# Performance work log

Hardware: AMD Instinct MI355X
Metric: run time of the kernel (lower is better)

The kernel has to match this reference:

```python
import jax, jax.numpy as jnp
import numpy as np

S, B, D, H = 2048, 64, 128, 128


def setup_inputs() -> dict:
    key = jax.random.key(0)
    ks = jax.random.split(key, 7)
    scale = 1.0 / np.sqrt(H)
    return {
        "input": jax.random.normal(ks[0], (S, B, D), dtype=jnp.float32),
        "time": jax.random.uniform(ks[1], (S, B, 1), dtype=jnp.float32),
        "W_ih": jax.random.normal(ks[2], (4 * H, D), dtype=jnp.float32) * scale,
        "W_hh": jax.random.normal(ks[3], (4 * H, H), dtype=jnp.float32) * scale,
        "b": jax.random.normal(ks[4], (4 * H,), dtype=jnp.float32) * scale,
        "w_t": jax.random.uniform(ks[5], (H,), dtype=jnp.float32),
        "b_t": jax.random.uniform(ks[6], (H,), dtype=jnp.float32),
    }


def reference(input, time, W_ih, W_hh, b, w_t, b_t):
    # ReverseLSTMLayer: run a time-conditioned LSTM cell over REVERSED time steps,
    # then re-reverse the stacked outputs. state starts at zeros (state=None).
    Bsz = input.shape[1]
    Hd = W_hh.shape[1]

    def step(state, xt):
        x, t = xt  # x: [B, D], t: [B, 1]
        h, c = state
        gates = x @ W_ih.T + h @ W_hh.T + b  # [B, 4H]
        i_, f_, g_, o_ = jnp.split(gates, 4, axis=-1)
        i_ = jax.nn.sigmoid(i_)
        f_ = jax.nn.sigmoid(f_)
        g_ = jnp.tanh(g_)
        o_ = jax.nn.sigmoid(o_)
        # learned exponential time decay on the carried cell state (T-LSTM style)
        decay = jnp.exp(-jax.nn.relu(t * w_t + b_t))  # [B, H]
        c = f_ * c * decay + i_ * g_
        h = o_ * jnp.tanh(c)
        return (h, c), h

    init = (jnp.zeros((Bsz, Hd), input.dtype), jnp.zeros((Bsz, Hd), input.dtype))
    # iterate over reversed sequence, then reverse outputs back
    (h, c), ys_rev = jax.lax.scan(step, init, (input[::-1], time[::-1]))
    outputs = ys_rev[::-1]  # [S, B, H]
    return outputs, (h, c)
```

## Files before the change

kernel.cpp:

```cpp
#include <hip/hip_runtime.h>

#define S_LEN 2048
#define B_SZ  64
#define D_IN  128
#define H_SZ  128
#define G4    512

typedef __attribute__((ext_vector_type(4))) float     floatx4;
typedef __attribute__((ext_vector_type(8))) _Float16  half8;
typedef __attribute__((ext_vector_type(2))) _Float16  half2_t;

union H8 { half8 v; half2_t p[4]; };

template<int CTRL>
__device__ __forceinline__ float qperm(float v) {
  return __int_as_float(
      __builtin_amdgcn_mov_dpp(__float_as_int(v), CTRL, 0xF, 0xF, true));
}

__global__ __launch_bounds__(256) void gx_gemm(
    const float* __restrict__ X,
    const float* __restrict__ Wih,
    const float* __restrict__ bias,
    _Float16* __restrict__ gx)
{
  __shared__ _Float16 Wl[128][136];
  const int tid  = threadIdx.x;
  const int lane = tid & 63;
  const int wv   = tid >> 6;
  const int R0   = blockIdx.x * 64;
  const int m    = lane & 15;
  const int q    = lane >> 4;

  half8 afrag[4];
  const float* xrow = X + (size_t)(R0 + wv * 16 + m) * D_IN;
  #pragma unroll
  for (int kf = 0; kf < 4; ++kf) {
    const int k0 = kf * 32 + q * 8;
    floatx4 v0 = *(const floatx4*)(xrow + k0);
    floatx4 v1 = *(const floatx4*)(xrow + k0 + 4);
    half8 a;
    a[0] = (_Float16)v0.x; a[1] = (_Float16)v0.y;
    a[2] = (_Float16)v0.z; a[3] = (_Float16)v0.w;
    a[4] = (_Float16)v1.x; a[5] = (_Float16)v1.y;
    a[6] = (_Float16)v1.z; a[7] = (_Float16)v1.w;
    afrag[kf] = a;
  }

  for (int nc = 0; nc < 4; ++nc) {
    __syncthreads();
    for (int i = tid; i < 128 * 32; i += 256) {
      const int row = i >> 5;
      const int c4  = (i & 31) * 4;
      floatx4 v = *(const floatx4*)(Wih + ((size_t)nc * 128 + row) * D_IN + c4);
      Wl[row][c4 + 0] = (_Float16)v.x;
      Wl[row][c4 + 1] = (_Float16)v.y;
      Wl[row][c4 + 2] = (_Float16)v.z;
      Wl[row][c4 + 3] = (_Float16)v.w;
    }
    __syncthreads();

    #pragma unroll
    for (int nt = 0; nt < 8; ++nt) {
      const int n0  = nc * 128 + nt * 16;
      const int nlo = nt * 16 + m;
      const float bv = bias[n0 + m];
      floatx4 acc = {bv, bv, bv, bv};
      #pragma unroll
      for (int kf = 0; kf < 4; ++kf) {
        half8 bfrag = *(const half8*)(&Wl[nlo][kf * 32 + q * 8]);
        acc = __builtin_amdgcn_mfma_f32_16x16x32_f16(afrag[kf], bfrag, acc,
                                                     0, 0, 0);
      }
      _Float16* gp = gx + (size_t)(R0 + wv * 16 + q * 4) * G4 + n0 + m;
      #pragma unroll
      for (int r = 0; r < 4; ++r) gp[(size_t)r * G4] = (_Float16)acc[r];
    }
  }
}

__global__ __launch_bounds__(512, 2) void lstm_rev(
    const _Float16* __restrict__ gx,
    const float* __restrict__ timep,
    const float* __restrict__ Whh,
    const float* __restrict__ w_t,
    const float* __restrict__ b_t,
    float* __restrict__ out)
{
  __shared__ __align__(16) _Float16 hbuf[2][H_SZ];
  const int tid = threadIdx.x;
  const int b   = blockIdx.x;
  const int tt  = tid & 3;
  const int col = tid >> 2;
  const int j   = tt * 128 + col;

  half8 w[4][4];
  #pragma unroll
  for (int ty = 0; ty < 4; ++ty) {
    const float* wrow = Whh + (size_t)(ty * 128 + col) * H_SZ + tt * 8;
    #pragma unroll
    for (int i = 0; i < 4; ++i) {
      floatx4 v0 = *(const floatx4*)(wrow + i * 32);
      floatx4 v1 = *(const floatx4*)(wrow + i * 32 + 4);
      half8 hh;
      hh[0] = (_Float16)v0.x; hh[1] = (_Float16)v0.y;
      hh[2] = (_Float16)v0.z; hh[3] = (_Float16)v0.w;
      hh[4] = (_Float16)v1.x; hh[5] = (_Float16)v1.y;
      hh[6] = (_Float16)v1.z; hh[7] = (_Float16)v1.w;
      w[ty][i] = hh;
    }
  }

  const float wt = w_t[col];
  const float bt = b_t[col];

  if (tid < H_SZ) hbuf[0][tid] = (_Float16)0.0f;
  __syncthreads();

  const float LOG2E  = 1.4426950408889634f;
  const float kscale = (tt == 2) ? (-2.0f * LOG2E) : (-LOG2E);
  const float am     = (tt == 2) ? 2.0f : 1.0f;
  const float aa     = (tt == 2) ? -1.0f : 0.0f;
  const bool  odd    = (tt & 1) != 0;

  float c = 0.0f;
  {
    const size_t idx0 = (size_t)(S_LEN - 1) * B_SZ + b;
    float gxc = (float)gx[idx0 * G4 + j];
    float tmc = timep[idx0];

    for (int t = S_LEN - 1; t >= 0; --t) {
      const int tn = (t > 0) ? (t - 1) : 0;
      const size_t idxn = (size_t)tn * B_SZ + b;
      const float gxn = (float)gx[idxn * G4 + j];
      const float tmn = timep[idxn];

      const int rb = (S_LEN - 1 - t) & 1;

      H8 hv[4];
      #pragma unroll
      for (int i = 0; i < 4; ++i)
        hv[i].v = *(const half8*)(&hbuf[rb][i * 32 + tt * 8]);

      float acc[4][2] = {{0.f,0.f},{0.f,0.f},{0.f,0.f},{0.f,0.f}};
      #pragma unroll
      for (int i = 0; i < 4; ++i) {
        H8 wu0; wu0.v = w[0][i];
        H8 wu1; wu1.v = w[1][i];
        H8 wu2; wu2.v = w[2][i];
        H8 wu3; wu3.v = w[3][i];
        #pragma unroll
        for (int p = 0; p < 4; ++p) {
          const int ch = p >> 1;
          acc[0][ch] = __builtin_amdgcn_fdot2(hv[i].p[p], wu0.p[p],
                                              acc[0][ch], false);
          acc[1][ch] = __builtin_amdgcn_fdot2(hv[i].p[p], wu1.p[p],
                                              acc[1][ch], false);
          acc[2][ch] = __builtin_amdgcn_fdot2(hv[i].p[p], wu2.p[p],
                                              acc[2][ch], false);
          acc[3][ch] = __builtin_amdgcn_fdot2(hv[i].p[p], wu3.p[p],
                                              acc[3][ch], false);
        }
      }
      float a0 = acc[0][0] + acc[0][1];
      float a1 = acc[1][0] + acc[1][1];
      float a2 = acc[2][0] + acc[2][1];
      float a3 = acc[3][0] + acc[3][1];

      a0 += qperm<0xB1>(a0); a0 += qperm<0x4E>(a0);
      a1 += qperm<0xB1>(a1); a1 += qperm<0x4E>(a1);
      a2 += qperm<0xB1>(a2); a2 += qperm<0x4E>(a2);
      a3 += qperm<0xB1>(a3); a3 += qperm<0x4E>(a3);

      float pre = (tt & 1) ? ((tt & 2) ? a3 : a1) : ((tt & 2) ? a2 : a0);
      pre += gxc;

      const float e = __builtin_amdgcn_exp2f(pre * kscale);
      const float v = fmaf(am, __builtin_amdgcn_rcpf(1.0f + e), aa);

      float z = fmaf(tmc, wt, bt);
      z = fmaxf(z, 0.0f);
      const float d = __builtin_amdgcn_exp2f(-LOG2E * z);

      const float p2 = qperm<0x4E>(v);
      const float fv = (tt == 1) ? v : p2;
      const float r  = odd ? fv * (d * c) : v * p2;
      const float cn = r + qperm<0xB1>(r);
      c = cn;

      const float e2 = __builtin_amdgcn_exp2f(-2.0f * LOG2E * cn);
      const float th = fmaf(2.0f, __builtin_amdgcn_rcpf(1.0f + e2), -1.0f);

      if (tt == 3) {
        const float h = v * th;
        hbuf[rb ^ 1][col] = (_Float16)h;
        out[((size_t)t * B_SZ + b) * H_SZ + col] = h;
        if (t == 0) {
          out[(size_t)S_LEN * B_SZ * H_SZ + (size_t)b * H_SZ + col] = h;
          out[(size_t)S_LEN * B_SZ * H_SZ + (size_t)B_SZ * H_SZ
              + (size_t)b * H_SZ + col] = c;
        }
      }
      __syncthreads();
      gxc = gxn; tmc = tmn;
    }
  }
}

extern "C" void kernel_launch(void* const* d_in, const int* in_sizes, int n_in,
                              void* d_out, int out_size, void* d_ws, size_t ws_size,
                              hipStream_t stream) {
  const float* input = (const float*)d_in[0];
  const float* timep = (const float*)d_in[1];
  const float* W_ih  = (const float*)d_in[2];
  const float* W_hh  = (const float*)d_in[3];
  const float* bias  = (const float*)d_in[4];
  const float* w_t   = (const float*)d_in[5];
  const float* b_t   = (const float*)d_in[6];
  float* out = (float*)d_out;

  _Float16* gx = (_Float16*)d_ws;

  gx_gemm<<<dim3((S_LEN * B_SZ) / 64), dim3(256), 0, stream>>>(
      input, W_ih, bias, gx);

  lstm_rev<<<dim3(B_SZ), dim3(512), 0, stream>>>(
      gx, timep, W_hh, w_t, b_t, out);
}
```

Baseline: 1.367 ms.

## Fold activation scales into weights, unroll recurrence by two, enlarge GEMM row tile

Pre-multiplies the sigmoid/tanh exponent scales into W_hh and the gx GEMM output, and folds -log2e into w_t/b_t, so the per-step pre-activation multiply disappears and relu plus negate becomes a single fmin. The recurrent loop is manually unrolled by two with static ping-pong LDS buffers and pointer-decrement addressing, and the barrier becomes s_waitcnt lgkmcnt(0) followed by s_barrier. The gx GEMM now processes 256 rows per block and reuses the LDS B fragments across four row groups. Scaling before the fp16 conversion slightly changes rounding and raises register pressure in the GEMM.

```diff
diff --git a/kernel.cpp b/kernel.cpp
--- a/kernel.cpp
+++ b/kernel.cpp
@@ -10,12 +10,19 @@
 typedef __attribute__((ext_vector_type(8))) _Float16  half8;
 typedef __attribute__((ext_vector_type(2))) _Float16  half2_t;
 
-union H8 { half8 v; half2_t p[4]; };
-
 template<int CTRL>
 __device__ __forceinline__ float qperm(float v) {
   return __int_as_float(
       __builtin_amdgcn_mov_dpp(__float_as_int(v), CTRL, 0xF, 0xF, true));
+}
+
+template<int P>
+__device__ __forceinline__ half2_t h2ext(half8 v) {
+  return __builtin_shufflevector(v, v, 2 * P, 2 * P + 1);
+}
+
+__device__ __forceinline__ void lds_barrier() {
+  asm volatile("s_waitcnt lgkmcnt(0)\n\ts_barrier" ::: "memory");
 }
 
 __global__ __launch_bounds__(256) void gx_gemm(
@@ -28,26 +35,32 @@
   const int tid  = threadIdx.x;
   const int lane = tid & 63;
   const int wv   = tid >> 6;
-  const int R0   = blockIdx.x * 64;
+  const int R0   = blockIdx.x * 256;
   const int m    = lane & 15;
   const int q    = lane >> 4;
 
-  half8 afrag[4];
-  const float* xrow = X + (size_t)(R0 + wv * 16 + m) * D_IN;
+  const float LOG2E = 1.4426950408889634f;
+
+  half8 afrag[4][4];
   #pragma unroll
-  for (int kf = 0; kf < 4; ++kf) {
-    const int k0 = kf * 32 + q * 8;
-    floatx4 v0 = *(const floatx4*)(xrow + k0);
-    floatx4 v1 = *(const floatx4*)(xrow + k0 + 4);
-    half8 a;
-    a[0] = (_Float16)v0.x; a[1] = (_Float16)v0.y;
-    a[2] = (_Float16)v0.z; a[3] = (_Float16)v0.w;
-    a[4] = (_Float16)v1.x; a[5] = (_Float16)v1.y;
-    a[6] = (_Float16)v1.z; a[7] = (_Float16)v1.w;
-    afrag[kf] = a;
+  for (int rg = 0; rg < 4; ++rg) {
+    const float* xrow = X + (size_t)(R0 + rg * 64 + wv * 16 + m) * D_IN;
+    #pragma unroll
+    for (int kf = 0; kf < 4; ++kf) {
+      const int k0 = kf * 32 + q * 8;
+      floatx4 v0 = *(const floatx4*)(xrow + k0);
+      floatx4 v1 = *(const floatx4*)(xrow + k0 + 4);
+      half8 a;
+      a[0] = (_Float16)v0.x; a[1] = (_Float16)v0.y;
+      a[2] = (_Float16)v0.z; a[3] = (_Float16)v0.w;
+      a[4] = (_Float16)v1.x; a[5] = (_Float16)v1.y;
+      a[6] = (_Float16)v1.z; a[7] = (_Float16)v1.w;
+      afrag[rg][kf] = a;
+    }
   }
 
   for (int nc = 0; nc < 4; ++nc) {
+    const float sc = (nc == 2) ? (-2.0f * LOG2E) : (-LOG2E);
     __syncthreads();
     for (int i = tid; i < 128 * 32; i += 256) {
       const int row = i >> 5;
@@ -65,26 +78,98 @@
       const int n0  = nc * 128 + nt * 16;
       const int nlo = nt * 16 + m;
       const float bv = bias[n0 + m];
-      floatx4 acc = {bv, bv, bv, bv};
+      half8 bfrag[4];
       #pragma unroll
-      for (int kf = 0; kf < 4; ++kf) {
-        half8 bfrag = *(const half8*)(&Wl[nlo][kf * 32 + q * 8]);
-        acc = __builtin_amdgcn_mfma_f32_16x16x32_f16(afrag[kf], bfrag, acc,
-                                                     0, 0, 0);
+      for (int kf = 0; kf < 4; ++kf)
+        bfrag[kf] = *(const half8*)(&Wl[nlo][kf * 32 + q * 8]);
+      #pragma unroll
+      for (int rg = 0; rg < 4; ++rg) {
+        floatx4 acc = {bv, bv, bv, bv};
+        #pragma unroll
+        for (int kf = 0; kf < 4; ++kf)
+          acc = __builtin_amdgcn_mfma_f32_16x16x32_f16(afrag[rg][kf],
+                                                       bfrag[kf], acc, 0, 0, 0);
+        _Float16* gp =
+            gx + (size_t)(R0 + rg * 64 + wv * 16 + q * 4) * G4 + n0 + m;
+        #pragma unroll
+        for (int r = 0; r < 4; ++r)
+          gp[(size_t)r * G4] = (_Float16)(acc[r] * sc);
       }
-      _Float16* gp = gx + (size_t)(R0 + wv * 16 + q * 4) * G4 + n0 + m;
-      #pragma unroll
-      for (int r = 0; r < 4; ++r) gp[(size_t)r * G4] = (_Float16)acc[r];
-    }
-  }
-}
+    }
+  }
+}
+
+#define LSTM_STEP(HR, HW, TCUR, GPN, TPN)                                     \
+  {                                                                           \
+    const float gxn = (float)*(GPN);                                          \
+    const float tmn = *(TPN);                                                 \
+    half8 hv0 = *(const half8*)((HR) + 0 * 32 + tt * 8);                      \
+    half8 hv1 = *(const half8*)((HR) + 1 * 32 + tt * 8);                      \
+    half8 hv2 = *(const half8*)((HR) + 2 * 32 + tt * 8);                      \
+    half8 hv3 = *(const half8*)((HR) + 3 * 32 + tt * 8);                      \
+    float q0a = 0.f, q0b = 0.f, q1a = 0.f, q1b = 0.f;                         \
+    float q2a = 0.f, q2b = 0.f, q3a = 0.f, q3b = 0.f;                         \
+    DOT8(0, hv0); DOT8(1, hv1); DOT8(2, hv2); DOT8(3, hv3);                   \
+    float a0 = q0a + q0b, a1 = q1a + q1b, a2 = q2a + q2b, a3 = q3a + q3b;     \
+    a0 += qperm<0xB1>(a0); a1 += qperm<0xB1>(a1);                             \
+    a2 += qperm<0xB1>(a2); a3 += qperm<0xB1>(a3);                             \
+    a0 += qperm<0x4E>(a0); a1 += qperm<0x4E>(a1);                             \
+    a2 += qperm<0x4E>(a2); a3 += qperm<0x4E>(a3);                             \
+    float pre = (tt & 1) ? ((tt & 2) ? a3 : a1) : ((tt & 2) ? a2 : a0);       \
+    pre += gxc;       \
+    const float e = __builtin_amdgcn_exp2f(pre);                              \
+    const float v = fmaf(am, __builtin_amdgcn_rcpf(1.0f + e), aa);            \
+    float z = fmaf(tmc, wt, bt);                    \
+    z = fminf(z, 0.0f);                                   \
+    const float d = __builtin_amdgcn_exp2f(z);                                \
+    const float p2 = qperm<0x4E>(v);                                          \
+    const float fv = (tt == 1) ? v : p2;                                      \
+    const float r  = odd ? fv * (d * c) : v * p2;                             \
+    const float cn = r + qperm<0xB1>(r);                                      \
+    c = cn;                                                                   \
+    const float e2 = __builtin_amdgcn_exp2f(-2.0f * LOG2E * cn);              \
+    const float th = fmaf(2.0f, __builtin_amdgcn_rcpf(1.0f + e2), -1.0f);     \
+    if (tt == 3) {                                                            \
+      const float h = v * th;                                                 \
+      (HW)[col] = (_Float16)h;                                                \
+      op[0] = h;                                                              \
+      if ((TCUR) == 0) {                                                      \
+        out[(size_t)S_LEN * B_SZ * H_SZ + (size_t)b * H_SZ + col] = h;        \
+        out[(size_t)S_LEN * B_SZ * H_SZ + (size_t)B_SZ * H_SZ                 \
+            + (size_t)b * H_SZ + col] = c;                                    \
+      }                                                                       \
+    }                                                                         \
+    lds_barrier();                                                            \
+    gxc = gxn; tmc = tmn;                                                     \
+    gp = (GPN); tp = (TPN); op -= (size_t)B_SZ * H_SZ;                        \
+  }
+
+#define DOT8(I, HV)                                                           \
+  {                                                                           \
+    q0a = __builtin_amdgcn_fdot2(h2ext<0>(HV), h2ext<0>(w[0][I]), q0a, false);\
+    q1a = __builtin_amdgcn_fdot2(h2ext<0>(HV), h2ext<0>(w[1][I]), q1a, false);\
+    q2a = __builtin_amdgcn_fdot2(h2ext<0>(HV), h2ext<0>(w[2][I]), q2a, false);\
+    q3a = __builtin_amdgcn_fdot2(h2ext<0>(HV), h2ext<0>(w[3][I]), q3a, false);\
+    q0a = __builtin_amdgcn_fdot2(h2ext<1>(HV), h2ext<1>(w[0][I]), q0a, false);\
+    q1a = __builtin_amdgcn_fdot2(h2ext<1>(HV), h2ext<1>(w[1][I]), q1a, false);\
+    q2a = __builtin_amdgcn_fdot2(h2ext<1>(HV), h2ext<1>(w[2][I]), q2a, false);\
+    q3a = __builtin_amdgcn_fdot2(h2ext<1>(HV), h2ext<1>(w[3][I]), q3a, false);\
+    q0b = __builtin_amdgcn_fdot2(h2ext<2>(HV), h2ext<2>(w[0][I]), q0b, false);\
+    q1b = __builtin_amdgcn_fdot2(h2ext<2>(HV), h2ext<2>(w[1][I]), q1b, false);\
+    q2b = __builtin_amdgcn_fdot2(h2ext<2>(HV), h2ext<2>(w[2][I]), q2b, false);\
+    q3b = __builtin_amdgcn_fdot2(h2ext<2>(HV), h2ext<2>(w[3][I]), q3b, false);\
+    q0b = __builtin_amdgcn_fdot2(h2ext<3>(HV), h2ext<3>(w[0][I]), q0b, false);\
+    q1b = __builtin_amdgcn_fdot2(h2ext<3>(HV), h2ext<3>(w[1][I]), q1b, false);\
+    q2b = __builtin_amdgcn_fdot2(h2ext<3>(HV), h2ext<3>(w[2][I]), q2b, false);\
+    q3b = __builtin_amdgcn_fdot2(h2ext<3>(HV), h2ext<3>(w[3][I]), q3b, false);\
+  }
 
 __global__ __launch_bounds__(512, 2) void lstm_rev(
     const _Float16* __restrict__ gx,
     const float* __restrict__ timep,
     const float* __restrict__ Whh,
-    const float* __restrict__ w_t,
-    const float* __restrict__ b_t,
+    const float* __restrict__ w_tp,
+    const float* __restrict__ b_tp,
     float* __restrict__ out)
 {
   __shared__ __align__(16) _Float16 hbuf[2][H_SZ];
@@ -94,115 +179,55 @@
   const int col = tid >> 2;
   const int j   = tt * 128 + col;
 
+  const float LOG2E = 1.4426950408889634f;
+
   half8 w[4][4];
   #pragma unroll
   for (int ty = 0; ty < 4; ++ty) {
+    const float sc = (ty == 2) ? (-2.0f * LOG2E) : (-LOG2E);
     const float* wrow = Whh + (size_t)(ty * 128 + col) * H_SZ + tt * 8;
     #pragma unroll
     for (int i = 0; i < 4; ++i) {
       floatx4 v0 = *(const floatx4*)(wrow + i * 32);
       floatx4 v1 = *(const floatx4*)(wrow + i * 32 + 4);
       half8 hh;
-      hh[0] = (_Float16)v0.x; hh[1] = (_Float16)v0.y;
-      hh[2] = (_Float16)v0.z; hh[3] = (_Float16)v0.w;
-      hh[4] = (_Float16)v1.x; hh[5] = (_Float16)v1.y;
-      hh[6] = (_Float16)v1.z; hh[7] = (_Float16)v1.w;
+      hh[0] = (_Float16)(v0.x * sc); hh[1] = (_Float16)(v0.y * sc);
+      hh[2] = (_Float16)(v0.z * sc); hh[3] = (_Float16)(v0.w * sc);
+      hh[4] = (_Float16)(v1.x * sc); hh[5] = (_Float16)(v1.y * sc);
+      hh[6] = (_Float16)(v1.z * sc); hh[7] = (_Float16)(v1.w * sc);
       w[ty][i] = hh;
     }
   }
 
-  const float wt = w_t[col];
-  const float bt = b_t[col];
+  const float wt = -LOG2E * w_tp[col];
+  const float bt = -LOG2E * b_tp[col];
+
+  const float kscale = (tt == 2) ? (-2.0f * LOG2E) : (-LOG2E);
+  (void)kscale;
+  const float am  = (tt == 2) ? 2.0f : 1.0f;
+  const float aa  = (tt == 2) ? -1.0f : 0.0f;
+  const bool  odd = (tt & 1) != 0;
 
   if (tid < H_SZ) hbuf[0][tid] = (_Float16)0.0f;
   __syncthreads();
 
-  const float LOG2E  = 1.4426950408889634f;
-  const float kscale = (tt == 2) ? (-2.0f * LOG2E) : (-LOG2E);
-  const float am     = (tt == 2) ? 2.0f : 1.0f;
-  const float aa     = (tt == 2) ? -1.0f : 0.0f;
-  const bool  odd    = (tt & 1) != 0;
-
+  const _Float16* gp = gx + ((size_t)(S_LEN - 1) * B_SZ + b) * G4 + j;
+  const float*    tp = timep + (size_t)(S_LEN - 1) * B_SZ + b;
+  float*          op = out + ((size_t)(S_LEN - 1) * B_SZ + b) * H_SZ + col;
+
+  float gxc = (float)*gp;
+  float tmc = *tp;
   float c = 0.0f;
-  {
-    const size_t idx0 = (size_t)(S_LEN - 1) * B_SZ + b;
-    float gxc = (float)gx[idx0 * G4 + j];
-    float tmc = timep[idx0];
-
-    for (int t = S_LEN - 1; t >= 0; --t) {
-      const int tn = (t > 0) ? (t - 1) : 0;
-      const size_t idxn = (size_t)tn * B_SZ + b;
-      const float gxn = (float)gx[idxn * G4 + j];
-      const float tmn = timep[idxn];
-
-      const int rb = (S_LEN - 1 - t) & 1;
-
-      H8 hv[4];
-      #pragma unroll
-      for (int i = 0; i < 4; ++i)
-        hv[i].v = *(const half8*)(&hbuf[rb][i * 32 + tt * 8]);
-
-      float acc[4][2] = {{0.f,0.f},{0.f,0.f},{0.f,0.f},{0.f,0.f}};
-      #pragma unroll
-      for (int i = 0; i < 4; ++i) {
-        H8 wu0; wu0.v = w[0][i];
-        H8 wu1; wu1.v = w[1][i];
-        H8 wu2; wu2.v = w[2][i];
-        H8 wu3; wu3.v = w[3][i];
-        #pragma unroll
-        for (int p = 0; p < 4; ++p) {
-          const int ch = p >> 1;
-          acc[0][ch] = __builtin_amdgcn_fdot2(hv[i].p[p], wu0.p[p],
-                                              acc[0][ch], false);
-          acc[1][ch] = __builtin_amdgcn_fdot2(hv[i].p[p], wu1.p[p],
-                                              acc[1][ch], false);
-          acc[2][ch] = __builtin_amdgcn_fdot2(hv[i].p[p], wu2.p[p],
-                                              acc[2][ch], false);
-          acc[3][ch] = __builtin_amdgcn_fdot2(hv[i].p[p], wu3.p[p],
-                                              acc[3][ch], false);
-        }
-      }
-      float a0 = acc[0][0] + acc[0][1];
-      float a1 = acc[1][0] + acc[1][1];
-      float a2 = acc[2][0] + acc[2][1];
-      float a3 = acc[3][0] + acc[3][1];
-
-      a0 += qperm<0xB1>(a0); a0 += qperm<0x4E>(a0);
-      a1 += qperm<0xB1>(a1); a1 += qperm<0x4E>(a1);
-      a2 += qperm<0xB1>(a2); a2 += qperm<0x4E>(a2);
-      a3 += qperm<0xB1>(a3); a3 += qperm<0x4E>(a3);
-
-      float pre = (tt & 1) ? ((tt & 2) ? a3 : a1) : ((tt & 2) ? a2 : a0);
-      pre += gxc;
-
-      const float e = __builtin_amdgcn_exp2f(pre * kscale);
-      const float v = fmaf(am, __builtin_amdgcn_rcpf(1.0f + e), aa);
-
-      float z = fmaf(tmc, wt, bt);
-      z = fmaxf(z, 0.0f);
-      const float d = __builtin_amdgcn_exp2f(-LOG2E * z);
-
-      const float p2 = qperm<0x4E>(v);
-      const float fv = (tt == 1) ? v : p2;
-      const float r  = odd ? fv * (d * c) : v * p2;
-      const float cn = r + qperm<0xB1>(r);
-      c = cn;
-
-      const float e2 = __builtin_amdgcn_exp2f(-2.0f * LOG2E * cn);
-      const float th = fmaf(2.0f, __builtin_amdgcn_rcpf(1.0f + e2), -1.0f);
-
-      if (tt == 3) {
-        const float h = v * th;
-        hbuf[rb ^ 1][col] = (_Float16)h;
-        out[((size_t)t * B_SZ + b) * H_SZ + col] = h;
-        if (t == 0) {
-          out[(size_t)S_LEN * B_SZ * H_SZ + (size_t)b * H_SZ + col] = h;
-          out[(size_t)S_LEN * B_SZ * H_SZ + (size_t)B_SZ * H_SZ
-              + (size_t)b * H_SZ + col] = c;
-        }
-      }
-      __syncthreads();
-      gxc = gxn; tmc = tmn;
+
+  _Float16* h0 = &hbuf[0][0];
+  _Float16* h1 = &hbuf[1][0];
+
+  for (int t = S_LEN - 1; t > 0; t -= 2) {
+    LSTM_STEP(h0, h1, t, gp - (size_t)B_SZ * G4, tp - B_SZ);
+    {
+      const _Float16* gpn = (t > 1) ? gp - (size_t)B_SZ * G4 : gp;
+      const float*    tpn = (t > 1) ? tp - B_SZ : tp;
+      LSTM_STEP(h1, h0, t - 1, gpn, tpn);
     }
   }
 }
@@ -221,7 +246,7 @@
 
   _Float16* gx = (_Float16*)d_ws;
 
-  gx_gemm<<<dim3((S_LEN * B_SZ) / 64), dim3(256), 0, stream>>>(
+  gx_gemm<<<dim3((S_LEN * B_SZ) / 256), dim3(256), 0, stream>>>(
       input, W_ih, bias, gx);
 
   lstm_rev<<<dim3(B_SZ), dim3(512), 0, stream>>>(
```

Measured after the change: 1.333 ms. 2.5% less time.
